# Performance work log

Measured on AMD Instinct MI355X. Metric: run time of the kernel, lower is better.

## Reference

```python
import jax, jax.numpy as jnp
import numpy as np

N_EMBD = 1024
N_HEAD = 16
HEAD_DIM = N_EMBD // N_HEAD
EPS = 1e-8


def rmsnorm(x, scale):
    return x * jax.lax.rsqrt(jnp.mean(x * x, axis=-1, keepdims=True) + EPS) * scale


def setup_inputs() -> dict:
    key = jax.random.key(0)
    ks = jax.random.split(key, 7)
    B, L, D = 4, 2048, N_EMBD
    s = lambda fan_in: 1.0 / np.sqrt(fan_in)
    return {
        "x": jax.random.normal(ks[0], (B, L, D), jnp.float32),
        "norm1_scale": jnp.ones((D,), jnp.float32),
        "w_qkv": jax.random.normal(ks[1], (D, 3 * D), jnp.float32) * s(D),
        "w_proj": jax.random.normal(ks[2], (D, D), jnp.float32) * s(D),
        "norm2_scale": jnp.ones((D,), jnp.float32),
        "w_fc1": jax.random.normal(ks[3], (D, 4 * D), jnp.float32) * s(D),
        "w_fc2": jax.random.normal(ks[4], (4 * D, D), jnp.float32) * s(4 * D),
    }


def reference(x, norm1_scale, w_qkv, w_proj, norm2_scale, w_fc1, w_fc2):
    B, L, D = x.shape
    H, hd = N_HEAD, HEAD_DIM

    # --- attention sub-block ---
    h = rmsnorm(x, norm1_scale)
    qkv = h @ w_qkv  # [B, L, 3D]
    q, k, v = jnp.split(qkv, 3, axis=-1)
    q = q.reshape(B, L, H, hd).transpose(0, 2, 1, 3)  # [B, H, L, hd]
    k = k.reshape(B, L, H, hd).transpose(0, 2, 1, 3)
    v = v.reshape(B, L, H, hd).transpose(0, 2, 1, 3)
    att = jnp.einsum("bhqd,bhkd->bhqk", q, k) * (hd ** -0.5)
    att = jax.nn.softmax(att, axis=-1)  # bidirectional, no mask
    out = jnp.einsum("bhqk,bhkd->bhqd", att, v)
    out = out.transpose(0, 2, 1, 3).reshape(B, L, D)
    x = x + out @ w_proj

    # --- MLP sub-block ---
    h = rmsnorm(x, norm2_scale)
    x = x + jax.nn.gelu(h @ w_fc1, approximate=False) @ w_fc2
    return x
```

## Files before the change

### kernel.cpp

```cpp
#include <hip/hip_runtime.h>
#include <hip/hip_bf16.h>
#include <cmath>


typedef __bf16 bf16x8 __attribute__((ext_vector_type(8)));
typedef __bf16 bf16x2 __attribute__((ext_vector_type(2)));
typedef float f32x4 __attribute__((ext_vector_type(4)));

__device__ __forceinline__ float bf2f(unsigned short u) {
  union { unsigned int i; float f; } c; c.i = ((unsigned int)u) << 16; return c.f;
}
__device__ __forceinline__ unsigned short f2bf(float f) {
  union { unsigned int i; float f; } c; c.f = f;
  unsigned int r = c.i + 0x7fffu + ((c.i >> 16) & 1u);
  return (unsigned short)(r >> 16);
}

__device__ __forceinline__ bool probe_bf16(const void* p) {
  return *reinterpret_cast<const unsigned int*>(p) == 0x3F803F80u;
}
__device__ __forceinline__ float ldext(const void* p, size_t i, bool isbf) {
  return isbf ? bf2f(reinterpret_cast<const unsigned short*>(p)[i])
              : reinterpret_cast<const float*>(p)[i];
}

__device__ __forceinline__ void cp16(const unsigned short* g, unsigned short* l) {
  __builtin_amdgcn_global_load_lds(
      (const __attribute__((address_space(1))) unsigned int*)g,
      (__attribute__((address_space(3))) unsigned int*)l,
      16, 0, 0);
}

__global__ __launch_bounds__(256) void transpose_any(
    const void* __restrict__ in, unsigned short* __restrict__ out,
    int R, int C, const void* __restrict__ probe) {
  const bool isbf = probe_bf16(probe);
  __shared__ unsigned short tile[32][33];
  const int bx = blockIdx.x * 32;
  const int by = blockIdx.y * 32;
  const int tx = threadIdx.x & 31, ty = threadIdx.x >> 5;
#pragma unroll
  for (int i = 0; i < 32; i += 8)
    tile[ty + i][tx] = f2bf(ldext(in, (size_t)(by + ty + i) * C + bx + tx, isbf));
  __syncthreads();
#pragma unroll
  for (int i = 0; i < 32; i += 8)
    out[(size_t)(bx + ty + i) * R + by + tx] = tile[tx][ty + i];
}

__device__ __forceinline__ void rmsnorm_body(
    const float v0, const float v1, const float v2, const float v3,
    const void* scale, bool isbf, unsigned short* outrow, int tid) {
  float ss = v0 * v0 + v1 * v1 + v2 * v2 + v3 * v3;
#pragma unroll
  for (int m = 32; m >= 1; m >>= 1) ss += __shfl_xor(ss, m);
  __shared__ float red[4];
  if ((tid & 63) == 0) red[tid >> 6] = ss;
  __syncthreads();
  ss = red[0] + red[1] + red[2] + red[3];
  const float rstd = rsqrtf(ss * (1.0f / 1024.0f) + 1e-8f);
  ushort4 o;
  o.x = f2bf(v0 * rstd * ldext(scale, tid * 4 + 0, isbf));
  o.y = f2bf(v1 * rstd * ldext(scale, tid * 4 + 1, isbf));
  o.z = f2bf(v2 * rstd * ldext(scale, tid * 4 + 2, isbf));
  o.w = f2bf(v3 * rstd * ldext(scale, tid * 4 + 3, isbf));
  reinterpret_cast<ushort4*>(outrow)[tid] = o;
}

__global__ __launch_bounds__(256) void rmsnorm_ext(
    const void* __restrict__ x, const void* __restrict__ scale,
    unsigned short* __restrict__ out, const void* __restrict__ probe) {
  const bool isbf = probe_bf16(probe);
  const int row = blockIdx.x, tid = threadIdx.x;
  float v0, v1, v2, v3;
  if (isbf) {
    ushort4 u = reinterpret_cast<const ushort4*>(x)[(size_t)row * 256 + tid];
    v0 = bf2f(u.x); v1 = bf2f(u.y); v2 = bf2f(u.z); v3 = bf2f(u.w);
  } else {
    float4 f = reinterpret_cast<const float4*>(x)[(size_t)row * 256 + tid];
    v0 = f.x; v1 = f.y; v2 = f.z; v3 = f.w;
  }
  rmsnorm_body(v0, v1, v2, v3, scale, isbf, out + (size_t)row * 1024, tid);
}

__global__ __launch_bounds__(256) void rmsnorm_int(
    const unsigned short* __restrict__ x, const void* __restrict__ scale,
    unsigned short* __restrict__ out, const void* __restrict__ probe) {
  const bool isbf = probe_bf16(probe);
  const int row = blockIdx.x, tid = threadIdx.x;
  ushort4 u = reinterpret_cast<const ushort4*>(x + (size_t)row * 1024)[tid];
  rmsnorm_body(bf2f(u.x), bf2f(u.y), bf2f(u.z), bf2f(u.w),
               scale, isbf, out + (size_t)row * 1024, tid);
}

#define PH_PRE { __builtin_amdgcn_s_barrier(); \
  asm volatile("s_waitcnt lgkmcnt(0)" ::: "memory"); \
  __builtin_amdgcn_sched_barrier(0); \
  __builtin_amdgcn_s_setprio(1); }
#define PH_POST { __builtin_amdgcn_s_setprio(0); __builtin_amdgcn_s_barrier(); }

#define LDA_(par, mh) \
  _Pragma("unroll") for (int mi = 0; mi < 4; ++mi) \
  _Pragma("unroll") for (int kk = 0; kk < 2; ++kk) \
    afr[mi][kk] = *reinterpret_cast<const bf16x8*>( \
        &As[par][mh][(wr * 64 + mi * 16 + l16) * 64 + ((((kk << 2) + quad) ^ (l16 & 7)) << 3)]);

#define LDB_(par, nh, dst) \
  _Pragma("unroll") for (int ni = 0; ni < 2; ++ni) \
  _Pragma("unroll") for (int kk = 0; kk < 2; ++kk) \
    dst[ni][kk] = *reinterpret_cast<const bf16x8*>( \
        &Bs[par][nh][(wc * 32 + ni * 16 + l16) * 64 + ((((kk << 2) + quad) ^ (l16 & 7)) << 3)]);

#define MM_(bfx, mh, nh) \
  _Pragma("unroll") for (int kk = 0; kk < 2; ++kk) \
  _Pragma("unroll") for (int mi = 0; mi < 4; ++mi) \
  _Pragma("unroll") for (int ni = 0; ni < 2; ++ni) \
    acc[(mh) * 4 + mi][(nh) * 2 + ni] = __builtin_amdgcn_mfma_f32_16x16x32_bf16( \
        afr[mi][kk], bfx[ni][kk], acc[(mh) * 4 + mi][(nh) * 2 + ni], 0, 0, 0);

#define SA_(par, hh, kt) { \
  cp16(A + oA[0][hh] + (kt), &As[par][hh][(w * 64) * 8]); \
  cp16(A + oA[1][hh] + (kt), &As[par][hh][(512 + w * 64) * 8]); }
#define SB_(par, hh, kt) { \
  cp16(BT + oB[0][hh] + (kt), &Bs[par][hh][(w * 64) * 8]); \
  cp16(BT + oB[1][hh] + (kt), &Bs[par][hh][(512 + w * 64) * 8]); }

#define TILE_(par, tt) { \
  const int kt1 = ((tt) + 1) << 6; \
  const int kt2 = ((tt) + 2) << 6; \
  LDA_(par, 0); LDB_(par, 0, bf0); \
  if (kt1 < K) SA_(par ^ 1, 1, kt1); \
  PH_PRE; MM_(bf0, 0, 0); PH_POST; \
  LDB_(par, 1, bf1); \
  if (kt2 < K) SA_(par, 0, kt2); \
  PH_PRE; MM_(bf1, 0, 1); PH_POST; \
  LDA_(par, 1); \
  if (kt2 < K) SB_(par, 0, kt2); \
  PH_PRE; MM_(bf1, 1, 1); PH_POST; \
  if (kt2 < K) SB_(par, 1, kt2); \
  PH_PRE; MM_(bf0, 1, 0); \
  __builtin_amdgcn_s_setprio(0); \
  if (kt2 < K)      { asm volatile("s_waitcnt vmcnt(6)" ::: "memory"); } \
  else if (kt1 < K) { asm volatile("s_waitcnt vmcnt(0)" ::: "memory"); } \
  if (kt1 < K) __builtin_amdgcn_s_barrier(); }

template <int EPI, typename OutT>
__global__ __launch_bounds__(512, 2) void gemm8p(
    const unsigned short* __restrict__ A, const unsigned short* __restrict__ BT,
    OutT* __restrict__ C, const void* __restrict__ Res,
    int M, int N, int K, const void* __restrict__ probe) {
  __shared__ __align__(16) unsigned short As[2][2][128 * 64];
  __shared__ __align__(16) unsigned short Bs[2][2][128 * 64];
  const int tid = threadIdx.x;
  const int lane = tid & 63;
  const int w = tid >> 6;
  const int quad = lane >> 4, l16 = lane & 15;
  const int wr = w >> 2, wc = w & 3;
  const int m0 = blockIdx.y * 256;
  const int n0 = blockIdx.x * 256;
  const int nt = K >> 6;

  size_t oA[2][2], oB[2][2];
#pragma unroll
  for (int i = 0; i < 2; ++i) {
    const int c = i * 512 + w * 64 + lane;
    const int r = c >> 3;
    const int gc = (c & 7) ^ (r & 7);
#pragma unroll
    for (int hh = 0; hh < 2; ++hh) {
      oA[i][hh] = (size_t)(m0 + hh * 128 + r) * K + gc * 8;
      oB[i][hh] = (size_t)(n0 + hh * 128 + r) * K + gc * 8;
    }
  }

  const f32x4 zero = {0.f, 0.f, 0.f, 0.f};
  f32x4 acc[8][4];
#pragma unroll
  for (int i = 0; i < 8; ++i)
#pragma unroll
    for (int j = 0; j < 4; ++j) acc[i][j] = zero;

  SA_(0, 0, 0); SB_(0, 0, 0); SB_(0, 1, 0); SA_(0, 1, 0);
  if (K > 64) {
    SA_(1, 0, 64); SB_(1, 0, 64); SB_(1, 1, 64);
    asm volatile("s_waitcnt vmcnt(6)" ::: "memory");
  } else {
    asm volatile("s_waitcnt vmcnt(0)" ::: "memory");
  }
  __builtin_amdgcn_s_barrier();

  bf16x8 afr[4][2], bf0[2][2], bf1[2][2];
  for (int t = 0; t < nt; t += 2) {
    TILE_(0, t);
    TILE_(1, t + 1);
  }

  if constexpr (EPI == 5) {
    if (n0 >= 2048) {
      unsigned short* vt = (unsigned short*)Res;
#pragma unroll
      for (int mh = 0; mh < 2; ++mh)
#pragma unroll
        for (int mi = 0; mi < 4; ++mi) {
          const int r0 = m0 + mh * 128 + wr * 64 + mi * 16 + quad * 4;
          const int bq = r0 >> 11;
          const int key = r0 & 2047;
#pragma unroll
          for (int nh = 0; nh < 2; ++nh)
#pragma unroll
            for (int ni = 0; ni < 2; ++ni) {
              const int vcol = n0 - 2048 + nh * 128 + wc * 32 + ni * 16 + l16;
              const f32x4 a4 = acc[mh * 4 + mi][nh * 2 + ni];
              ushort4 o4;
              o4.x = f2bf(a4[0]); o4.y = f2bf(a4[1]);
              o4.z = f2bf(a4[2]); o4.w = f2bf(a4[3]);
              *reinterpret_cast<ushort4*>(
                  vt + (((size_t)(bq * 1024 + vcol)) << 11) + key) = o4;
            }
        }
      return;
    }
  }

#pragma unroll
  for (int mh = 0; mh < 2; ++mh)
#pragma unroll
    for (int mi = 0; mi < 4; ++mi)
#pragma unroll
      for (int reg = 0; reg < 4; ++reg) {
        const int row = m0 + mh * 128 + wr * 64 + mi * 16 + quad * 4 + reg;
#pragma unroll
        for (int nh = 0; nh < 2; ++nh)
#pragma unroll
          for (int ni = 0; ni < 2; ++ni) {
            const int col = n0 + nh * 128 + wc * 32 + ni * 16 + l16;
            float v = acc[mh * 4 + mi][nh * 2 + ni][reg];
            if (EPI == 1) v = 0.5f * v * (1.0f + erff(v * 0.70710678118654752f));
            if (EPI == 5 && col < 1024) v *= 0.18033688011112042f;
            if constexpr (sizeof(OutT) == 2)
              C[(size_t)row * N + col] = f2bf(v);
            else
              C[(size_t)row * N + col] = v;
          }
      }
}

template <int EPI, typename OutT>
__global__ __launch_bounds__(256) void gemm_bt(
    const unsigned short* __restrict__ A, const unsigned short* __restrict__ BT,
    OutT* __restrict__ C, const void* __restrict__ Res,
    int M, int N, int K, const void* __restrict__ probe) {
  __shared__ __align__(16) unsigned short As[128 * 64];
  __shared__ __align__(16) unsigned short Bs[128 * 64];
  const int tid = threadIdx.x;
  const int lane = tid & 63;
  const int w = tid >> 6;
  const int quad = lane >> 4;
  const int l16 = lane & 15;
  const int wr = w >> 1, wc = w & 1;
  const int m0 = blockIdx.y * 128;
  const int n0 = blockIdx.x * 128;

  const f32x4 zero = {0.f, 0.f, 0.f, 0.f};
  f32x4 acc[4][4];
#pragma unroll
  for (int i = 0; i < 4; ++i)
#pragma unroll
    for (int j = 0; j < 4; ++j) acc[i][j] = zero;

  for (int kt = 0; kt < K; kt += 64) {
#pragma unroll
    for (int i = 0; i < 4; ++i) {
      const int cb = (i * 4 + w) * 64;
      const int c = cb + lane;
      const int row = c >> 3;
      const int gc = (c & 7) ^ (row & 7);
      cp16(A + (size_t)(m0 + row) * K + kt + gc * 8, As + (size_t)cb * 8);
      cp16(BT + (size_t)(n0 + row) * K + kt + gc * 8, Bs + (size_t)cb * 8);
    }
    __syncthreads();

#pragma unroll
    for (int kk = 0; kk < 2; ++kk) {
      bf16x8 af[4], bfr[4];
#pragma unroll
      for (int mi = 0; mi < 4; ++mi)
        af[mi] = *reinterpret_cast<const bf16x8*>(
            As + (wr * 64 + mi * 16 + l16) * 64 + ((((kk << 2) + quad) ^ (l16 & 7)) << 3));
#pragma unroll
      for (int ni = 0; ni < 4; ++ni)
        bfr[ni] = *reinterpret_cast<const bf16x8*>(
            Bs + (wc * 64 + ni * 16 + l16) * 64 + ((((kk << 2) + quad) ^ (l16 & 7)) << 3));
#pragma unroll
      for (int mi = 0; mi < 4; ++mi)
#pragma unroll
        for (int ni = 0; ni < 4; ++ni)
          acc[mi][ni] = __builtin_amdgcn_mfma_f32_16x16x32_bf16(af[mi], bfr[ni], acc[mi][ni], 0, 0, 0);
    }
    __syncthreads();
  }

  const bool pb = (EPI == 3) ? probe_bf16(probe) : true;
#pragma unroll
  for (int mi = 0; mi < 4; ++mi) {
#pragma unroll
    for (int reg = 0; reg < 4; ++reg) {
      const int row = m0 + wr * 64 + mi * 16 + quad * 4 + reg;
#pragma unroll
      for (int ni = 0; ni < 4; ++ni) {
        const int col = n0 + wc * 64 + ni * 16 + l16;
        float v = acc[mi][ni][reg];
        if (EPI == 1) v = 0.5f * v * (1.0f + erff(v * 0.70710678118654752f));
        if (EPI == 2) v += bf2f(reinterpret_cast<const unsigned short*>(Res)[(size_t)row * N + col]);
        if (EPI == 3) v += ldext(Res, (size_t)row * N + col, pb);
        if constexpr (sizeof(OutT) == 2)
          C[(size_t)row * N + col] = f2bf(v);
        else
          C[(size_t)row * N + col] = v;
      }
    }
  }
}

__global__ __launch_bounds__(256) void flash_attn(
    const unsigned short* __restrict__ qkv,
    const unsigned short* __restrict__ vT,
    unsigned short* __restrict__ out) {
  __shared__ __align__(16) unsigned short Ks[2][64 * 64];
  __shared__ __align__(16) unsigned short Vs[2][64 * 64];
  const int L = 2048, DQ = 3072, D = 1024;
  const int qt = blockIdx.x, h = blockIdx.y, b = blockIdx.z;
  const int tid = threadIdx.x, lane = tid & 63, w = tid >> 6;
  const int quad = lane >> 4, l16 = lane & 15;
  const int woff = w * 32;
  const unsigned short* base = qkv + (size_t)b * L * DQ;
  const unsigned short* vbase = vT + (size_t)(b * 1024 + h * 64) * 2048;

  unsigned short* Qs = &Vs[0][0];
#pragma unroll
  for (int i = 0; i < 4; ++i) {
    const int cb = i * 256 + w * 64;
    const int c = cb + lane;
    const int r = c >> 3, d8 = (c & 7) << 3;
    cp16(base + (size_t)(qt * 128 + r) * DQ + h * 64 + d8, Qs + ((size_t)cb << 3));
  }
  asm volatile("s_waitcnt vmcnt(0)" ::: "memory");
  __builtin_amdgcn_s_barrier();
  __builtin_amdgcn_sched_barrier(0);
  bf16x8 qf[2][2];
#pragma unroll
  for (int mj = 0; mj < 2; ++mj)
#pragma unroll
    for (int kc = 0; kc < 2; ++kc)
      qf[mj][kc] = *reinterpret_cast<const bf16x8*>(
          Qs + (woff + mj * 16 + l16) * 64 + kc * 32 + quad * 8);
  asm volatile("s_waitcnt lgkmcnt(0)" ::: "memory");
  __builtin_amdgcn_sched_barrier(0);
  __builtin_amdgcn_s_barrier();

  auto STAGE = [&](int s, int kt0) {
#pragma unroll
    for (int i = 0; i < 2; ++i) {
      const int cb = i * 256 + w * 64;
      const int cd = cb + lane;
      const int m = cd >> 3, cc = cd & 7;
      const int gk = ((m >> 4) & 1) * 32 + ((m >> 2) & 3) * 8 + (m >> 5) * 4 + (m & 3);
      const int gc = cc ^ (m & 7);
      cp16(base + (size_t)(kt0 + gk) * DQ + 1024 + h * 64 + gc * 8,
           &Ks[s][(size_t)cb << 3]);
    }
#pragma unroll
    for (int i = 0; i < 2; ++i) {
      const int cb = i * 256 + w * 64;
      const int cd = cb + lane;
      const int d = cd >> 3, cc = cd & 7;
      const int gc = cc ^ (d & 7);
      cp16(vbase + (size_t)d * 2048 + kt0 + gc * 8, &Vs[s][(size_t)cb << 3]);
    }
  };

  STAGE(0, 0);

  const f32x4 zero = {0.f, 0.f, 0.f, 0.f};
  f32x4 l4[2] = {zero, zero};
  f32x4 o[2][4];
#pragma unroll
  for (int mj = 0; mj < 2; ++mj)
#pragma unroll
    for (int nd = 0; nd < 4; ++nd) o[mj][nd] = zero;

  for (int kt = 0; kt < L; kt += 64) {
    const int cur = (kt >> 6) & 1;
    if (kt + 64 < L) {
      STAGE(cur ^ 1, kt + 64);
      asm volatile("s_waitcnt vmcnt(4)" ::: "memory");
    } else {
      asm volatile("s_waitcnt vmcnt(0)" ::: "memory");
    }
    __builtin_amdgcn_s_barrier();
    __builtin_amdgcn_sched_barrier(0);

    f32x4 sv[4][2];
#pragma unroll
    for (int ki = 0; ki < 4; ++ki)
#pragma unroll
      for (int mj = 0; mj < 2; ++mj) sv[ki][mj] = zero;
#pragma unroll
    for (int kc = 0; kc < 2; ++kc) {
      bf16x8 kf[4];
#pragma unroll
      for (int ki = 0; ki < 4; ++ki)
        kf[ki] = *reinterpret_cast<const bf16x8*>(
            &Ks[cur][(ki * 16 + l16) * 64 + ((((kc << 2) + quad) ^ (l16 & 7)) << 3)]);
      __builtin_amdgcn_s_setprio(1);
#pragma unroll
      for (int ki = 0; ki < 4; ++ki)
#pragma unroll
        for (int mj = 0; mj < 2; ++mj)
          sv[ki][mj] = __builtin_amdgcn_mfma_f32_16x16x32_bf16(kf[ki], qf[mj][kc], sv[ki][mj], 0, 0, 0);
      __builtin_amdgcn_s_setprio(0);
    }

    bf16x8 pf[2][2];
#pragma unroll
    for (int mj = 0; mj < 2; ++mj)
#pragma unroll
      for (int kc = 0; kc < 2; ++kc) {
        f32x4 pa, pb;
#pragma unroll
        for (int r = 0; r < 4; ++r) pa[r] = __builtin_amdgcn_exp2f(sv[kc][mj][r]);
#pragma unroll
        for (int r = 0; r < 4; ++r) pb[r] = __builtin_amdgcn_exp2f(sv[kc + 2][mj][r]);
        l4[mj] += pa;
        l4[mj] += pb;
        bf16x8 t;
        t[0] = (__bf16)pa[0]; t[1] = (__bf16)pa[1]; t[2] = (__bf16)pa[2]; t[3] = (__bf16)pa[3];
        t[4] = (__bf16)pb[0]; t[5] = (__bf16)pb[1]; t[6] = (__bf16)pb[2]; t[7] = (__bf16)pb[3];
        pf[mj][kc] = t;
      }

#pragma unroll
    for (int kc = 0; kc < 2; ++kc) {
      bf16x8 vf[4];
#pragma unroll
      for (int nd = 0; nd < 4; ++nd)
        vf[nd] = *reinterpret_cast<const bf16x8*>(
            &Vs[cur][(nd * 16 + l16) * 64 + ((((kc << 2) + quad) ^ (l16 & 7)) << 3)]);
      __builtin_amdgcn_s_setprio(1);
#pragma unroll
      for (int mj = 0; mj < 2; ++mj)
#pragma unroll
        for (int nd = 0; nd < 4; ++nd)
          o[mj][nd] = __builtin_amdgcn_mfma_f32_16x16x32_bf16(pf[mj][kc], vf[nd], o[mj][nd], 0, 0, 0);
      __builtin_amdgcn_s_setprio(0);
    }

    if (kt + 64 < L) {
      asm volatile("s_waitcnt lgkmcnt(0)" ::: "memory");
      __builtin_amdgcn_sched_barrier(0);
      __builtin_amdgcn_s_barrier();
    }
  }

#pragma unroll
  for (int mj = 0; mj < 2; ++mj) {
    float lp = l4[mj][0] + l4[mj][1] + l4[mj][2] + l4[mj][3];
    lp += __shfl_xor(lp, 16);
    lp += __shfl_xor(lp, 32);
#pragma unroll
    for (int r = 0; r < 4; ++r) {
      const float inv = 1.0f / __shfl(lp, quad * 4 + r);
      const int row = qt * 128 + woff + mj * 16 + quad * 4 + r;
#pragma unroll
      for (int nd = 0; nd < 4; ++nd) {
        const int col = h * 64 + nd * 16 + l16;
        out[(size_t)(b * L + row) * D + col] = f2bf(o[mj][nd][r] * inv);
      }
    }
  }
}

extern "C" void kernel_launch(void* const* d_in, const int* in_sizes, int n_in,
                              void* d_out, int out_size, void* d_ws, size_t ws_size,
                              hipStream_t stream) {
  const void* x      = d_in[0];
  const void* n1s    = d_in[1];
  const void* w_qkv  = d_in[2];
  const void* w_proj = d_in[3];
  const void* n2s    = d_in[4];
  const void* w_fc1  = d_in[5];
  const void* w_fc2  = d_in[6];
  float* out = (float*)d_out;
  char* ws = (char*)d_ws;

  const int M = 8192;
  unsigned short* wqkvT  = (unsigned short*)(ws + ((size_t)0   << 20));
  unsigned short* wprojT = (unsigned short*)(ws + ((size_t)6   << 20));
  unsigned short* wfc1T  = (unsigned short*)(ws + ((size_t)8   << 20));
  unsigned short* wfc2T  = (unsigned short*)(ws + ((size_t)16  << 20));
  unsigned short* h      = (unsigned short*)(ws + ((size_t)24  << 20));
  unsigned short* qkvb   = (unsigned short*)(ws + ((size_t)40  << 20));
  unsigned short* attn   = (unsigned short*)(ws + ((size_t)88  << 20));
  unsigned short* x2     = (unsigned short*)(ws + ((size_t)104 << 20));
  unsigned short* g      = qkvb;
  unsigned short* vT     = x2;

  transpose_any<<<dim3(96, 32), 256, 0, stream>>>(w_qkv, wqkvT, 1024, 3072, n1s);
  transpose_any<<<dim3(32, 32), 256, 0, stream>>>(w_proj, wprojT, 1024, 1024, n1s);
  transpose_any<<<dim3(128, 32), 256, 0, stream>>>(w_fc1, wfc1T, 1024, 4096, n1s);
  transpose_any<<<dim3(32, 128), 256, 0, stream>>>(w_fc2, wfc2T, 4096, 1024, n1s);

  rmsnorm_ext<<<M, 256, 0, stream>>>(x, n1s, h, n1s);
  gemm8p<5, unsigned short><<<dim3(12, 32), 512, 0, stream>>>(h, wqkvT, qkvb, vT, M, 3072, 1024, n1s);
  flash_attn<<<dim3(16, 16, 4), 256, 0, stream>>>(qkvb, vT, attn);
  gemm_bt<3, unsigned short><<<dim3(8, 64), 256, 0, stream>>>(attn, wprojT, x2, x, M, 1024, 1024, n1s);
  rmsnorm_int<<<M, 256, 0, stream>>>(x2, n2s, h, n1s);
  gemm8p<1, unsigned short><<<dim3(16, 32), 512, 0, stream>>>(h, wfc1T, g, nullptr, M, 4096, 1024, n1s);
  gemm_bt<2, float><<<dim3(8, 64), 256, 0, stream>>>(g, wfc2T, out, x2, M, 1024, 4096, n1s);
}
```

Baseline: 561.1 us.

## Restructure GEMM main-loop schedule and remap blocks for XCD-aware L2 locality

Rewrites the 8-wave GEMM inner tile from four barrier-separated phases into two larger phases. All fragments for one half are loaded, then 16 MFMAs run, then all global prefetches are issued together. The loop is peeled into main and tail variants, so the per-tile K bounds checks go away. Both GEMM kernels also remap the block index so consecutive blocks on the same XCD work on M-adjacent tiles, which is meant to improve L2 reuse. The peeling assumes nt is at least 2 and even, and the remap assumes the grid size is divisible by 8.

```diff
diff --git a/kernel.cpp b/kernel.cpp
--- a/kernel.cpp
+++ b/kernel.cpp
@@ -93,16 +93,14 @@
                scale, isbf, out + (size_t)row * 1024, tid);
 }
 
-#define PH_PRE { __builtin_amdgcn_s_barrier(); \
-  asm volatile("s_waitcnt lgkmcnt(0)" ::: "memory"); \
-  __builtin_amdgcn_sched_barrier(0); \
-  __builtin_amdgcn_s_setprio(1); }
-#define PH_POST { __builtin_amdgcn_s_setprio(0); __builtin_amdgcn_s_barrier(); }
-
-#define LDA_(par, mh) \
+#define SB0 __builtin_amdgcn_sched_barrier(0)
+#define LGKM(n) asm volatile("s_waitcnt lgkmcnt(" #n ")" ::: "memory")
+#define VMC(n) asm volatile("s_waitcnt vmcnt(" #n ")" ::: "memory")
+
+#define LDA_(par, mh, dst) \
   _Pragma("unroll") for (int mi = 0; mi < 4; ++mi) \
   _Pragma("unroll") for (int kk = 0; kk < 2; ++kk) \
-    afr[mi][kk] = *reinterpret_cast<const bf16x8*>( \
+    dst[mi][kk] = *reinterpret_cast<const bf16x8*>( \
         &As[par][mh][(wr * 64 + mi * 16 + l16) * 64 + ((((kk << 2) + quad) ^ (l16 & 7)) << 3)]);
 
 #define LDB_(par, nh, dst) \
@@ -111,12 +109,12 @@
     dst[ni][kk] = *reinterpret_cast<const bf16x8*>( \
         &Bs[par][nh][(wc * 32 + ni * 16 + l16) * 64 + ((((kk << 2) + quad) ^ (l16 & 7)) << 3)]);
 
-#define MM_(bfx, mh, nh) \
+#define MM16_(af, bfx, mh, nh) \
   _Pragma("unroll") for (int kk = 0; kk < 2; ++kk) \
   _Pragma("unroll") for (int mi = 0; mi < 4; ++mi) \
   _Pragma("unroll") for (int ni = 0; ni < 2; ++ni) \
     acc[(mh) * 4 + mi][(nh) * 2 + ni] = __builtin_amdgcn_mfma_f32_16x16x32_bf16( \
-        afr[mi][kk], bfx[ni][kk], acc[(mh) * 4 + mi][(nh) * 2 + ni], 0, 0, 0);
+        af[mi][kk], bfx[ni][kk], acc[(mh) * 4 + mi][(nh) * 2 + ni], 0, 0, 0);
 
 #define SA_(par, hh, kt) { \
   cp16(A + oA[0][hh] + (kt), &As[par][hh][(w * 64) * 8]); \
@@ -125,24 +123,50 @@
   cp16(BT + oB[0][hh] + (kt), &Bs[par][hh][(w * 64) * 8]); \
   cp16(BT + oB[1][hh] + (kt), &Bs[par][hh][(512 + w * 64) * 8]); }
 
-#define TILE_(par, tt) { \
-  const int kt1 = ((tt) + 1) << 6; \
-  const int kt2 = ((tt) + 2) << 6; \
-  LDA_(par, 0); LDB_(par, 0, bf0); \
-  if (kt1 < K) SA_(par ^ 1, 1, kt1); \
-  PH_PRE; MM_(bf0, 0, 0); PH_POST; \
-  LDB_(par, 1, bf1); \
-  if (kt2 < K) SA_(par, 0, kt2); \
-  PH_PRE; MM_(bf1, 0, 1); PH_POST; \
-  LDA_(par, 1); \
-  if (kt2 < K) SB_(par, 0, kt2); \
-  PH_PRE; MM_(bf1, 1, 1); PH_POST; \
-  if (kt2 < K) SB_(par, 1, kt2); \
-  PH_PRE; MM_(bf0, 1, 0); \
-  __builtin_amdgcn_s_setprio(0); \
-  if (kt2 < K)      { asm volatile("s_waitcnt vmcnt(6)" ::: "memory"); } \
-  else if (kt1 < K) { asm volatile("s_waitcnt vmcnt(0)" ::: "memory"); } \
-  if (kt1 < K) __builtin_amdgcn_s_barrier(); }
+#define TILE_MAIN(par, tt) { \
+  LDA_(par, 0, afrA); LDB_(par, 0, bf0); LDB_(par, 1, bf1); SB0; \
+  LGKM(0); SB0; \
+  __builtin_amdgcn_s_setprio(1); \
+  MM16_(afrA, bf0, 0, 0); MM16_(afrA, bf1, 0, 1); \
+  __builtin_amdgcn_s_setprio(0); SB0; \
+  LDA_(par, 1, afrB); SB0; \
+  __builtin_amdgcn_s_barrier(); SB0; \
+  { const int kt1 = ((tt) + 1) << 6, kt2 = ((tt) + 2) << 6; \
+    SA_(par ^ 1, 1, kt1); SA_(par, 0, kt2); SB_(par, 0, kt2); SB_(par, 1, kt2); } SB0; \
+  LGKM(0); SB0; \
+  __builtin_amdgcn_s_setprio(1); \
+  MM16_(afrB, bf1, 1, 1); MM16_(afrB, bf0, 1, 0); \
+  __builtin_amdgcn_s_setprio(0); SB0; \
+  VMC(6); SB0; \
+  __builtin_amdgcn_s_barrier(); }
+
+#define TILE_T1(par, tt) { \
+  LDA_(par, 0, afrA); LDB_(par, 0, bf0); LDB_(par, 1, bf1); SB0; \
+  LGKM(0); SB0; \
+  __builtin_amdgcn_s_setprio(1); \
+  MM16_(afrA, bf0, 0, 0); MM16_(afrA, bf1, 0, 1); \
+  __builtin_amdgcn_s_setprio(0); SB0; \
+  LDA_(par, 1, afrB); SB0; \
+  __builtin_amdgcn_s_barrier(); SB0; \
+  { const int kt1 = ((tt) + 1) << 6; SA_(par ^ 1, 1, kt1); } SB0; \
+  LGKM(0); SB0; \
+  __builtin_amdgcn_s_setprio(1); \
+  MM16_(afrB, bf1, 1, 1); MM16_(afrB, bf0, 1, 0); \
+  __builtin_amdgcn_s_setprio(0); SB0; \
+  VMC(0); SB0; \
+  __builtin_amdgcn_s_barrier(); }
+
+#define TILE_T2(par) { \
+  LDA_(par, 0, afrA); LDB_(par, 0, bf0); LDB_(par, 1, bf1); SB0; \
+  LGKM(0); SB0; \
+  __builtin_amdgcn_s_setprio(1); \
+  MM16_(afrA, bf0, 0, 0); MM16_(afrA, bf1, 0, 1); \
+  __builtin_amdgcn_s_setprio(0); SB0; \
+  LDA_(par, 1, afrB); SB0; \
+  LGKM(0); SB0; \
+  __builtin_amdgcn_s_setprio(1); \
+  MM16_(afrB, bf1, 1, 1); MM16_(afrB, bf0, 1, 0); \
+  __builtin_amdgcn_s_setprio(0); }
 
 template <int EPI, typename OutT>
 __global__ __launch_bounds__(512, 2) void gemm8p(
@@ -156,8 +180,12 @@
   const int w = tid >> 6;
   const int quad = lane >> 4, l16 = lane & 15;
   const int wr = w >> 2, wc = w & 3;
-  const int m0 = blockIdx.y * 256;
-  const int n0 = blockIdx.x * 256;
+
+  const int gx = gridDim.x, gy = gridDim.y;
+  int lin = blockIdx.y * gx + blockIdx.x;
+  lin = (lin & 7) * ((gx * gy) >> 3) + (lin >> 3);
+  const int m0 = (lin % gy) * 256;
+  const int n0 = (lin / gy) * 256;
   const int nt = K >> 6;
 
   size_t oA[2][2], oB[2][2];
@@ -181,19 +209,17 @@
     for (int j = 0; j < 4; ++j) acc[i][j] = zero;
 
   SA_(0, 0, 0); SB_(0, 0, 0); SB_(0, 1, 0); SA_(0, 1, 0);
-  if (K > 64) {
-    SA_(1, 0, 64); SB_(1, 0, 64); SB_(1, 1, 64);
-    asm volatile("s_waitcnt vmcnt(6)" ::: "memory");
-  } else {
-    asm volatile("s_waitcnt vmcnt(0)" ::: "memory");
-  }
+  SA_(1, 0, 64); SB_(1, 0, 64); SB_(1, 1, 64);
+  VMC(6); SB0;
   __builtin_amdgcn_s_barrier();
 
-  bf16x8 afr[4][2], bf0[2][2], bf1[2][2];
-  for (int t = 0; t < nt; t += 2) {
-    TILE_(0, t);
-    TILE_(1, t + 1);
-  }
+  bf16x8 afrA[4][2], afrB[4][2], bf0[2][2], bf1[2][2];
+  for (int t = 0; t + 2 < nt; t += 2) {
+    TILE_MAIN(0, t);
+    TILE_MAIN(1, t + 1);
+  }
+  TILE_T1(0, nt - 2);
+  TILE_T2(1);
 
   if constexpr (EPI == 5) {
     if (n0 >= 2048) {
@@ -258,8 +284,12 @@
   const int quad = lane >> 4;
   const int l16 = lane & 15;
   const int wr = w >> 1, wc = w & 1;
-  const int m0 = blockIdx.y * 128;
-  const int n0 = blockIdx.x * 128;
+
+  const int gx = gridDim.x, gy = gridDim.y;
+  int lin = blockIdx.y * gx + blockIdx.x;
+  lin = (lin & 7) * ((gx * gy) >> 3) + (lin >> 3);
+  const int m0 = (lin % gy) * 128;
+  const int n0 = (lin / gy) * 128;
 
   const f32x4 zero = {0.f, 0.f, 0.f, 0.f};
   f32x4 acc[4][4];
```

Result: faster. 548.8 us (-2.2%).
